# Performance work log

Hardware: AMD Instinct MI355X
Metric: run time of the kernel (lower is better)

The kernel has to match this reference:

```python
import jax, jax.numpy as jnp
import numpy as np
from jax import lax

B, N = 16, 2048
S0, S1, K = 256, 128, 32
EPS = 1e-5


def bn_relu(x, gamma, beta, axes):
    # training-mode BatchNorm (batch statistics) + ReLU; channel is last dim
    mean = jnp.mean(x, axis=axes, keepdims=True)
    var = jnp.var(x, axis=axes, keepdims=True)
    return jax.nn.relu((x - mean) * lax.rsqrt(var + EPS) * gamma + beta)


def fps(coords, s):
    # farthest point sampling, deterministic start at index 0. coords [B,N,3]
    b, n, _ = coords.shape
    def body(carry, _):
        dist, far = carry
        centroid = jnp.take_along_axis(coords, far[:, None, None], axis=1)  # [B,1,3]
        d = jnp.sum((coords - centroid) ** 2, axis=-1)                      # [B,N]
        dist = jnp.minimum(dist, d)
        return (dist, jnp.argmax(dist, axis=-1).astype(jnp.int32)), far
    init = (jnp.full((b, n), 1e10, coords.dtype), jnp.zeros((b,), jnp.int32))
    _, idx = lax.scan(body, init, None, length=s)
    return jnp.transpose(idx)  # [B,s]


def gather_points(pts, idx):
    # pts [B,N,C], idx [B,...] int -> [B,...,C]
    flat = idx.reshape(idx.shape[0], -1)[..., None]  # [B,M,1]
    out = jnp.take_along_axis(pts, flat, axis=1)     # [B,M,C]
    return out.reshape(*idx.shape, pts.shape[-1])


def sample_and_knn_group(s, k, coords, features):
    # coords [B,N,3], features [B,N,C] -> new_xyz [B,s,3], agg [B,s,k,2C]
    fps_idx = fps(coords, s)
    new_xyz = gather_points(coords, fps_idx)      # [B,s,3]
    center = gather_points(features, fps_idx)     # [B,s,C]
    d2 = jnp.sum((new_xyz[:, :, None, :] - coords[:, None, :, :]) ** 2, axis=-1)  # [B,s,N]
    _, knn_idx = lax.top_k(-d2, k)                # k smallest distances
    grouped = gather_points(features, knn_idx)    # [B,s,k,C]
    agg = jnp.concatenate(
        [grouped - center[:, :, None, :],
         jnp.broadcast_to(center[:, :, None, :], grouped.shape)], axis=-1)
    return new_xyz, agg


def sg_block(coords, features, s, k, w, gamma, beta):
    # conv1x1 -> BN -> ReLU -> max over k neighbors
    new_xyz, nf = sample_and_knn_group(s, k, coords, features)  # nf [B,s,k,d]
    h = jnp.einsum('bskd,od->bsko', nf, w)
    h = bn_relu(h, gamma, beta, axes=(0, 1, 2))
    return new_xyz, jnp.max(h, axis=2)  # [B,s,out]


def setup_inputs() -> dict:
    key = jax.random.key(0)
    ks = jax.random.split(key, 5)
    return {
        'x': jax.random.normal(ks[0], (B, 3, N), jnp.float32),
        'w1': jax.random.normal(ks[1], (64, 3), jnp.float32) * (1.0 / np.sqrt(3)),
        'g1': jnp.ones((64,), jnp.float32), 'b1': jnp.zeros((64,), jnp.float32),
        'w2': jax.random.normal(ks[2], (64, 64), jnp.float32) * 0.125,
        'g2': jnp.ones((64,), jnp.float32), 'b2': jnp.zeros((64,), jnp.float32),
        'w_sg0': jax.random.normal(ks[3], (128, 128), jnp.float32) * (1.0 / np.sqrt(128)),
        'g_sg0': jnp.ones((128,), jnp.float32), 'b_sg0': jnp.zeros((128,), jnp.float32),
        'w_sg1': jax.random.normal(ks[4], (256, 256), jnp.float32) * (1.0 / np.sqrt(256)),
        'g_sg1': jnp.ones((256,), jnp.float32), 'b_sg1': jnp.zeros((256,), jnp.float32),
    }


def reference(x, w1, g1, b1, w2, g2, b2, w_sg0, g_sg0, b_sg0, w_sg1, g_sg1, b_sg1):
    coords = jnp.transpose(x, (0, 2, 1))                   # [B,N,3]
    f = bn_relu(jnp.einsum('bnc,oc->bno', coords, w1), g1, b1, axes=(0, 1))  # [B,N,64]
    f = bn_relu(jnp.einsum('bnc,oc->bno', f, w2), g2, b2, axes=(0, 1))       # [B,N,64]
    xyz1, f1 = sg_block(coords, f, S0, K, w_sg0, g_sg0, b_sg0)   # [B,S0,128]
    _, f2 = sg_block(xyz1, f1, S1, K, w_sg1, g_sg1, b_sg1)       # [B,S1,256]
    return jnp.transpose(f2, (0, 2, 1))                           # [B,256,S1]
```

## Files before the change

### kernel.cpp

```cpp
#include <hip/hip_runtime.h>
#include <float.h>

#define BATCH 16
#define NPTS  2048
#define NS0   256
#define NS1   128
#define KK    32
#define EPSV  1e-5f
#define MROWS 32768.0f

__device__ __forceinline__ float sqdist(float ax,float ay,float az,float bx,float by,float bz){
  float dx=__fsub_rn(ax,bx), dy=__fsub_rn(ay,by), dz=__fsub_rn(az,bz);
  return __fadd_rn(__fadd_rn(__fmul_rn(dx,dx),__fmul_rn(dy,dy)),__fmul_rn(dz,dz));
}

template<int CTRL,int RM>
__device__ __forceinline__ float dpp_fmax_s(float x){
  int t = __builtin_amdgcn_update_dpp((int)0xFF800000, __float_as_int(x), CTRL, RM, 0xf, false);
  return fmaxf(x, __int_as_float(t));
}
template<int CTRL,int RM>
__device__ __forceinline__ float dpp_fmin_s(float x){
  int t = __builtin_amdgcn_update_dpp(0x7F800000, __float_as_int(x), CTRL, RM, 0xf, false);
  return fminf(x, __int_as_float(t));
}
template<int CTRL,int RM>
__device__ __forceinline__ unsigned dpp_umin_s(unsigned x){
  unsigned t = (unsigned)__builtin_amdgcn_update_dpp(-1, (int)x, CTRL, RM, 0xf, false);
  return t<x ? t : x;
}
__device__ __forceinline__ void wave_argmax_f32(float v, unsigned idx, float& mall, int& sel){
  float m=v;
  m=dpp_fmax_s<0x111,0xf>(m); m=dpp_fmax_s<0x112,0xf>(m); m=dpp_fmax_s<0x114,0xf>(m);
  m=dpp_fmax_s<0x118,0xf>(m); m=dpp_fmax_s<0x142,0xa>(m); m=dpp_fmax_s<0x143,0xc>(m);
  mall = __int_as_float(__builtin_amdgcn_readlane(__float_as_int(m),63));
  unsigned c = (v==mall)? idx : 0xFFFFFFFFu;
  c=dpp_umin_s<0x111,0xf>(c); c=dpp_umin_s<0x112,0xf>(c); c=dpp_umin_s<0x114,0xf>(c);
  c=dpp_umin_s<0x118,0xf>(c); c=dpp_umin_s<0x142,0xa>(c); c=dpp_umin_s<0x143,0xc>(c);
  sel = (int)(unsigned)__builtin_amdgcn_readlane((int)c,63);
}
__device__ __forceinline__ int wave_argmin_f32(float v, unsigned idx){
  float m=v;
  m=dpp_fmin_s<0x111,0xf>(m); m=dpp_fmin_s<0x112,0xf>(m); m=dpp_fmin_s<0x114,0xf>(m);
  m=dpp_fmin_s<0x118,0xf>(m); m=dpp_fmin_s<0x142,0xa>(m); m=dpp_fmin_s<0x143,0xc>(m);
  float mall = __int_as_float(__builtin_amdgcn_readlane(__float_as_int(m),63));
  unsigned c = (v==mall)? idx : 0xFFFFFFFFu;
  c=dpp_umin_s<0x111,0xf>(c); c=dpp_umin_s<0x112,0xf>(c); c=dpp_umin_s<0x114,0xf>(c);
  c=dpp_umin_s<0x118,0xf>(c); c=dpp_umin_s<0x142,0xa>(c); c=dpp_umin_s<0x143,0xc>(c);
  return (int)(unsigned)__builtin_amdgcn_readlane((int)c,63);
}


__device__ void embed1_body(int bid, const float* __restrict__ x, const float* __restrict__ w1,
                            float* __restrict__ coords, float* __restrict__ t1){
  __shared__ float w[64*3];
  int tid = threadIdx.x;
  if (tid < 192) w[tid] = w1[tid];
  __syncthreads();
  int gid = bid*256 + tid;
  int b = gid / NPTS, n = gid % NPTS;
  float cx = x[(b*3+0)*NPTS + n];
  float cy = x[(b*3+1)*NPTS + n];
  float cz = x[(b*3+2)*NPTS + n];
  coords[gid*3+0]=cx; coords[gid*3+1]=cy; coords[gid*3+2]=cz;
  float* o = t1 + (size_t)gid*64;
  #pragma unroll
  for(int j=0;j<64;j++) o[j] = cx*w[j*3+0] + cy*w[j*3+1] + cz*w[j*3+2];
}

__device__ void wt_body(int gid, const float* __restrict__ w0, float* __restrict__ wt0,
                        const float* __restrict__ w1, float* __restrict__ wt1){
  if(gid < 128*128){
    int o = gid % 128, c = gid / 128;
    wt0[gid] = w0[o*128 + c];
  } else {
    int g2 = gid - 128*128;
    if(g2 >= 256*256) return;
    int o = g2 % 256, c = g2 / 256;
    wt1[g2] = w1[o*256 + c];
  }
}

__device__ void statsA_body(int blk, const float* __restrict__ t,
                            float* __restrict__ accS, float* __restrict__ accQ){
  int c = threadIdx.x;
  int r0 = blk*128;
  float s=0.f, q=0.f;
  for(int r=0;r<128;r++){
    float v = t[(size_t)(r0+r)*64 + c];
    s+=v; q+=v*v;
  }
  atomicAdd(accS+c, s);
  atomicAdd(accQ+c, q);
}

__device__ void embed2_body(int bid, const float* __restrict__ t1, const float* __restrict__ w2,
                            const float* __restrict__ accS, const float* __restrict__ accQ,
                            const float* __restrict__ g1, const float* __restrict__ b1,
                            float* __restrict__ t2, char* smem){
  float (*fin)[64] = (float(*)[64])smem;
  float* sm = (float*)smem + 4096;
  float* sr = sm+64; float* sg = sr+64; float* sb = sg+64;
  int tid = threadIdx.x;
  if (tid<64){
    float S=accS[tid], Q=accQ[tid];
    float m = S/MROWS, v = Q/MROWS - m*m; if(v<0.f) v=0.f;
    sm[tid]=m; sr[tid]=rsqrtf(v+EPSV); sg[tid]=g1[tid]; sb[tid]=b1[tid];
  }
  __syncthreads();
  int base = bid*64;
  for(int i=tid;i<4096;i+=256){
    int p=i>>6, c=i&63;
    float v = t1[(size_t)(base+p)*64 + c];
    v = (v - sm[c])*sr[c]*sg[c] + sb[c];
    fin[p][c] = v>0.f ? v : 0.f;
  }
  __syncthreads();
  int o = tid & 63, p0 = tid>>6;
  float acc[16];
  #pragma unroll
  for(int i=0;i<16;i++) acc[i]=0.f;
  for(int cc=0; cc<64; cc+=4){
    float4 wv = *(const float4*)(w2 + o*64 + cc);
    #pragma unroll
    for(int i=0;i<16;i++){
      float4 f4 = *(const float4*)&fin[p0 + i*4][cc];
      acc[i] += f4.x*wv.x + f4.y*wv.y + f4.z*wv.z + f4.w*wv.w;
    }
  }
  #pragma unroll
  for(int i=0;i<16;i++) t2[(size_t)(base+p0+i*4)*64 + o] = acc[i];
}

template<int P, int S, int T>
__device__ void fps_body(int b, const float* __restrict__ x, int* __restrict__ outIdx,
                         float* __restrict__ outXyz, char* smem){
  constexpr int PPT = P/T;
  constexpr int NW  = T/64;
  float* sx=(float*)smem; float* sy=sx+P; float* sz=sy+P;
  int* sidx=(int*)(sz+P);
  unsigned long long* rv64=(unsigned long long*)(sidx+S);
  int tid = threadIdx.x;
  const float* xb = x + (size_t)b*3*P;
  float px[PPT], py[PPT], pz[PPT], dist[PPT];
  #pragma unroll
  for(int i=0;i<PPT;i++){
    int n = i*T + tid;
    float X=xb[n], Y=xb[P+n], Z=xb[2*P+n];
    px[i]=X; py[i]=Y; pz[i]=Z; dist[i]=1e10f;
    sx[n]=X; sy[n]=Y; sz[n]=Z;
  }
  __syncthreads();
  int cur = 0;
  float cx=sx[0], cy=sy[0], cz=sz[0];
  for(int s=0;s<S;s++){
    if(tid==0) sidx[s]=cur;
    if(s==S-1) break;
    float bv=-FLT_MAX; int bi=0;
    #pragma unroll
    for(int i=0;i<PPT;i++){
      float d = sqdist(px[i],py[i],pz[i],cx,cy,cz);
      float nd = fminf(dist[i], d);
      dist[i]=nd;
      int n = i*T + tid;
      if(nd>bv){ bv=nd; bi=n; }
    }
    float mall; int sel;
    wave_argmax_f32(bv,(unsigned)bi,mall,sel);
    int sl = s & 1;
    if((tid&63)==0) rv64[sl*NW+(tid>>6)] = ((unsigned long long)__float_as_uint(mall)<<32)|(unsigned)(~sel);
    __syncthreads();
    unsigned long long wk = rv64[sl*NW];
    #pragma unroll
    for(int w=1;w<NW;w++){ unsigned long long t = rv64[sl*NW+w]; if(t>wk) wk=t; }
    cur = (int)(~(unsigned)wk);
    cx=sx[cur]; cy=sy[cur]; cz=sz[cur];
  }
  __syncthreads();
  for(int i=tid; i<S; i+=T){
    int id = sidx[i];
    outIdx[b*S+i] = id;
    outXyz[((size_t)b*S+i)*3+0] = sx[id];
    outXyz[((size_t)b*S+i)*3+1] = sy[id];
    outXyz[((size_t)b*S+i)*3+2] = sz[id];
  }
}

template<int P, int S>
__device__ void fps_wave_body(int b, const float* __restrict__ pts, int* __restrict__ outIdx,
                              float* __restrict__ outXyz, char* smem){
  constexpr int PPT = P/64;
  float* sx=(float*)smem; float* sy=sx+P; float* sz=sy+P;
  int* sidx=(int*)(sz+P);
  int lane = threadIdx.x;
  const float* p = pts + (size_t)b*P*3;
  float px[PPT], py[PPT], pz[PPT], dist[PPT];
  #pragma unroll
  for(int i=0;i<PPT;i++){
    int n = i*64 + lane;
    float X=p[n*3], Y=p[n*3+1], Z=p[n*3+2];
    px[i]=X; py[i]=Y; pz[i]=Z; dist[i]=1e10f;
    sx[n]=X; sy[n]=Y; sz[n]=Z;
  }
  __syncthreads();
  int cur = 0;
  float cx=sx[0], cy=sy[0], cz=sz[0];
  for(int s=0;s<S;s++){
    if(lane==0) sidx[s]=cur;
    if(s==S-1) break;
    float bv=-FLT_MAX; int bi=0;
    #pragma unroll
    for(int i=0;i<PPT;i++){
      float d = sqdist(px[i],py[i],pz[i],cx,cy,cz);
      float nd = fminf(dist[i], d);
      dist[i]=nd;
      int n = i*64 + lane;
      if(nd>bv){ bv=nd; bi=n; }
    }
    float mall; int sel;
    wave_argmax_f32(bv,(unsigned)bi,mall,sel);
    cur = sel;
    cx=sx[cur]; cy=sy[cur]; cz=sz[cur];
  }
  __syncthreads();
  for(int i=lane; i<S; i+=64){
    int id = sidx[i];
    outIdx[b*S+i] = id;
    outXyz[((size_t)b*S+i)*3+0] = sx[id];
    outXyz[((size_t)b*S+i)*3+1] = sy[id];
    outXyz[((size_t)b*S+i)*3+2] = sz[id];
  }
}

template<int P>
__device__ void knn_body(int bq, const float* __restrict__ pts, const float* __restrict__ q,
                         int S, int* __restrict__ knn, char* smem){
  float* d2 = (float*)smem;
  constexpr int E = P/64;
  int lane = threadIdx.x;
  int b = bq / S;
  const float* p = pts + (size_t)b*P*3;
  float qx=q[(size_t)bq*3], qy=q[(size_t)bq*3+1], qz=q[(size_t)bq*3+2];
  #pragma unroll
  for(int i=0;i<E;i++){ int n=i*64+lane; d2[n] = sqdist(qx,qy,qz,p[n*3],p[n*3+1],p[n*3+2]); }
  __syncthreads();
  for(int j=0;j<KK;j++){
    float mv=FLT_MAX; unsigned mi=0xFFFFFFFFu;
    #pragma unroll
    for(int i=0;i<E;i++){
      int n=i*64+lane;
      float v=d2[n];
      if(v<mv){ mv=v; mi=(unsigned)n; }
    }
    int sel = wave_argmin_f32(mv, mi);
    if(lane==0){ knn[(size_t)bq*KK+j]=sel; d2[sel]=FLT_MAX; }
    __syncthreads();
  }
}

template<int C, int P, bool BN>
__device__ void pass1_body(int bq, const float* __restrict__ feats, const int* __restrict__ knn,
                           const int* __restrict__ fpsIdx, const float* __restrict__ WT,
                           float* __restrict__ hmax, float* __restrict__ hmin,
                           float* __restrict__ part, int S,
                           const float* __restrict__ accS, const float* __restrict__ accQ,
                           const float* __restrict__ bg, const float* __restrict__ bb){
  constexpr int O   = 2*C;
  constexpr int TPB = C;
  constexpr int C4  = C/4;
  constexpr int OG  = O/8;
  constexpr int LDC = C+4;
  __shared__ __align__(16) float gfp[KK*LDC];
  __shared__ __align__(16) float cf[C];
  __shared__ __align__(16) float sa[BN?C:1], sbb[BN?C:1];
  __shared__ float sct[O];
  __shared__ float xst[(TPB>64)? 8*O : 1];
  int tid = threadIdx.x;
  int b = bq / S;
  const float* fb = feats + (size_t)b*P*C;
  int ci = fpsIdx[bq];
  const float* cfg = fb + (size_t)ci*C;
  if(BN){
    float S_=accS[tid], Q_=accQ[tid];
    float m = S_/MROWS, vv = Q_/MROWS - m*m; if(vv<0.f) vv=0.f;
    float a = rsqrtf(vv+EPSV)*bg[tid];
    float sh = bb[tid] - m*a;
    sa[tid]=a; sbb[tid]=sh;
    float cv = a*cfg[tid] + sh;
    cf[tid] = cv>0.f ? cv : 0.f;
    __syncthreads();
  } else {
    cf[tid] = cfg[tid];
  }
  for(int i=tid; i<KK*C4; i+=TPB){
    int k = i/C4, d4 = i - k*C4;
    float4 g = ((const float4*)(fb + (size_t)knn[(size_t)bq*KK+k]*C))[d4];
    float4 r;
    if(BN){
      float4 a4 = *(const float4*)&sa[d4*4];
      float4 s4 = *(const float4*)&sbb[d4*4];
      float4 c4 = *(const float4*)&cf[d4*4];
      float gx = a4.x*g.x+s4.x; gx = gx>0.f?gx:0.f;
      float gy = a4.y*g.y+s4.y; gy = gy>0.f?gy:0.f;
      float gz = a4.z*g.z+s4.z; gz = gz>0.f?gz:0.f;
      float gw = a4.w*g.w+s4.w; gw = gw>0.f?gw:0.f;
      r.x=gx-c4.x; r.y=gy-c4.y; r.z=gz-c4.z; r.w=gw-c4.w;
    } else {
      float4 c4 = ((const float4*)cfg)[d4];
      r.x=g.x-c4.x; r.y=g.y-c4.y; r.z=g.z-c4.z; r.w=g.w-c4.w;
    }
    *(float4*)&gfp[k*LDC + d4*4] = r;
  }
  __syncthreads();
  {
    int o2 = tid*2;
    float ct0=0.f, ct1=0.f;
    for(int c=0;c<C;c+=4){
      float4 c4 = *(const float4*)&cf[c];
      #pragma unroll
      for(int t=0;t<4;t++){
        float cv = ((const float*)&c4)[t];
        float2 wh = *(const float2*)&WT[(size_t)(C+c+t)*O + o2];
        ct0 += cv*wh.x; ct1 += cv*wh.y;
      }
    }
    sct[o2]=ct0; sct[o2+1]=ct1;
  }
  __syncthreads();
  int kg = tid / OG;
  int og = tid % OG;
  float acc[8][8];
  #pragma unroll
  for(int a=0;a<8;a++)
    #pragma unroll
    for(int bb2=0;bb2<8;bb2++) acc[a][bb2]=0.f;
  for(int dc=0; dc<C4; dc++){
    float4 g4[8];
    #pragma unroll
    for(int jk=0;jk<8;jk++) g4[jk] = *(const float4*)&gfp[(kg*8+jk)*LDC + dc*4];
    #pragma unroll
    for(int t=0;t<4;t++){
      const float* wrow = WT + (size_t)(dc*4+t)*O + og*8;
      float4 wa = *(const float4*)wrow;
      float4 wb = *(const float4*)(wrow+4);
      #pragma unroll
      for(int jk=0;jk<8;jk++){
        float gs = ((const float*)&g4[jk])[t];
        acc[jk][0] += gs*wa.x; acc[jk][1] += gs*wa.y; acc[jk][2] += gs*wa.z; acc[jk][3] += gs*wa.w;
        acc[jk][4] += gs*wb.x; acc[jk][5] += gs*wb.y; acc[jk][6] += gs*wb.z; acc[jk][7] += gs*wb.w;
      }
    }
  }
  float tmx[8],tmn[8],tsm[8],tsq[8];
  #pragma unroll
  for(int jo=0;jo<8;jo++){
    int o = og*8+jo;
    float ct = sct[o];
    float s=0.f,q=0.f,mx=-FLT_MAX,mn=FLT_MAX;
    #pragma unroll
    for(int jk=0;jk<8;jk++){
      float h = acc[jk][jo] + ct;
      s+=h; q+=h*h; mx=fmaxf(mx,h); mn=fminf(mn,h);
    }
    tmx[jo]=mx; tmn[jo]=mn; tsm[jo]=s; tsq[jo]=q;
  }
  if constexpr (TPB==64){
    #pragma unroll
    for(int jo=0;jo<8;jo++){
      tmx[jo]=fmaxf(tmx[jo],__shfl_xor(tmx[jo],16)); tmx[jo]=fmaxf(tmx[jo],__shfl_xor(tmx[jo],32));
      tmn[jo]=fminf(tmn[jo],__shfl_xor(tmn[jo],16)); tmn[jo]=fminf(tmn[jo],__shfl_xor(tmn[jo],32));
      tsm[jo]+=__shfl_xor(tsm[jo],16); tsm[jo]+=__shfl_xor(tsm[jo],32);
      tsq[jo]+=__shfl_xor(tsq[jo],16); tsq[jo]+=__shfl_xor(tsq[jo],32);
    }
    if(tid<OG){
      #pragma unroll
      for(int jo=0;jo<8;jo++){
        int o = tid*8+jo;
        hmax[(size_t)bq*O+o]=tmx[jo]; hmin[(size_t)bq*O+o]=tmn[jo];
        part[(size_t)bq*2*O+o]=tsm[jo]; part[(size_t)bq*2*O+O+o]=tsq[jo];
      }
    }
  } else {
    #pragma unroll
    for(int jo=0;jo<8;jo++){
      tmx[jo]=fmaxf(tmx[jo],__shfl_xor(tmx[jo],32));
      tmn[jo]=fminf(tmn[jo],__shfl_xor(tmn[jo],32));
      tsm[jo]+=__shfl_xor(tsm[jo],32);
      tsq[jo]+=__shfl_xor(tsq[jo],32);
    }
    int wv = tid>>6;
    if((tid&63)<32){
      int og_ = tid&31;
      #pragma unroll
      for(int jo=0;jo<8;jo++){
        int o = og_*8+jo;
        xst[0*2*O + wv*O + o]=tmx[jo];
        xst[1*2*O + wv*O + o]=tmn[jo];
        xst[2*2*O + wv*O + o]=tsm[jo];
        xst[3*2*O + wv*O + o]=tsq[jo];
      }
    }
    __syncthreads();
    if(tid<32){
      #pragma unroll
      for(int jo=0;jo<8;jo++){
        int o = tid*8+jo;
        hmax[(size_t)bq*O+o]=fmaxf(xst[0*2*O+o], xst[0*2*O+O+o]);
        hmin[(size_t)bq*O+o]=fminf(xst[1*2*O+o], xst[1*2*O+O+o]);
        part[(size_t)bq*2*O+o]   = xst[2*2*O+o] + xst[2*2*O+O+o];
        part[(size_t)bq*2*O+O+o] = xst[3*2*O+o] + xst[3*2*O+O+o];
      }
    }
  }
}


__global__ __launch_bounds__(256) void k_embed1_wt(const float* __restrict__ x, const float* __restrict__ w1,
                         float* __restrict__ coords, float* __restrict__ t1,
                         const float* __restrict__ wsg0, float* __restrict__ wt0,
                         const float* __restrict__ wsg1, float* __restrict__ wt1,
                         float* __restrict__ accz){
  if(blockIdx.x < 128) embed1_body(blockIdx.x, x, w1, coords, t1);
  else if(blockIdx.x < 448) wt_body((blockIdx.x-128)*256 + threadIdx.x, wsg0, wt0, wsg1, wt1);
  else accz[threadIdx.x] = 0.f;
}

__global__ __launch_bounds__(64) void k_statsA(const float* __restrict__ t,
                         float* __restrict__ accS, float* __restrict__ accQ){
  statsA_body(blockIdx.x, t, accS, accQ);
}

__global__ __launch_bounds__(256, 1) void k_fps0_embed2(const float* __restrict__ x,
                         int* __restrict__ fps0, float* __restrict__ xyz0,
                         const float* __restrict__ t1, const float* __restrict__ w2,
                         const float* __restrict__ acc1S, const float* __restrict__ acc1Q,
                         const float* __restrict__ g1, const float* __restrict__ b1,
                         float* __restrict__ t2){
  extern __shared__ char smem[];
  if(blockIdx.x < BATCH) fps_body<NPTS,NS0,256>(blockIdx.x, x, fps0, xyz0, smem);
  else embed2_body(blockIdx.x-BATCH, t1, w2, acc1S, acc1Q, g1, b1, t2, smem);
}

__global__ __launch_bounds__(64, 4) void k_fps1_knn0_st2(const float* __restrict__ xyz0,
                         int* __restrict__ fps1, float* __restrict__ xyz1,
                         const float* __restrict__ coords, int* __restrict__ knn0,
                         const float* __restrict__ t2,
                         float* __restrict__ acc2S, float* __restrict__ acc2Q){
  extern __shared__ char smem[];
  if(blockIdx.x < BATCH) fps_wave_body<NS0,NS1>(blockIdx.x, xyz0, fps1, xyz1, smem);
  else if(blockIdx.x < BATCH + BATCH*NS0) knn_body<NPTS>(blockIdx.x-BATCH, coords, xyz0, NS0, knn0, smem);
  else statsA_body(blockIdx.x - (BATCH + BATCH*NS0), t2, acc2S, acc2Q);
}

__global__ __launch_bounds__(64, 2) void k_pass1a_knn1(const float* __restrict__ t2,
                         const int* __restrict__ knn0, const int* __restrict__ fps0,
                         const float* __restrict__ wt0,
                         float* __restrict__ hmax0, float* __restrict__ hmin0, float* __restrict__ part0,
                         const float* __restrict__ acc2S, const float* __restrict__ acc2Q,
                         const float* __restrict__ g2, const float* __restrict__ b2,
                         const float* __restrict__ xyz0, const float* __restrict__ xyz1,
                         int* __restrict__ knn1){
  extern __shared__ char smem[];
  if(blockIdx.x < BATCH*NS0)
    pass1_body<64,NPTS,true>(blockIdx.x, t2, knn0, fps0, wt0, hmax0, hmin0, part0, NS0,
                             acc2S, acc2Q, g2, b2);
  else
    knn_body<NS0>(blockIdx.x-BATCH*NS0, xyz0, xyz1, NS1, knn1, smem);
}

__global__ __launch_bounds__(128, 2) void k_pass1b(const float* __restrict__ f1,
                         const int* __restrict__ knn1, const int* __restrict__ fps1,
                         const float* __restrict__ wt1,
                         float* __restrict__ hmax1, float* __restrict__ hmin1, float* __restrict__ part1){
  pass1_body<128,NS0,false>(blockIdx.x, f1, knn1, fps1, wt1, hmax1, hmin1, part1, NS1,
                            nullptr, nullptr, nullptr, nullptr);
}

__global__ __launch_bounds__(256) void k_redpost0(const float* __restrict__ part,
        const float* __restrict__ hmax, const float* __restrict__ hmin,
        const float* __restrict__ g, const float* __restrict__ bb, float* __restrict__ f1){
  constexpr int O=128; constexpr int NB=BATCH*NS0;
  int o = blockIdx.x, tid = threadIdx.x;
  float s=0.f, s2=0.f;
  for(int i=tid;i<NB;i+=256){ s += part[(size_t)i*2*O+o]; s2 += part[(size_t)i*2*O+O+o]; }
  __shared__ float bs[256], bq[256];
  __shared__ float s_sc, s_sh;
  bs[tid]=s; bq[tid]=s2; __syncthreads();
  for(int st=128; st>0; st>>=1){ if(tid<st){ bs[tid]+=bs[tid+st]; bq[tid]+=bq[tid+st]; } __syncthreads(); }
  if(tid==0){
    float M = (float)(NB*KK);
    float m = bs[0]/M;
    float v = bq[0]/M - m*m; if(v<0.f) v=0.f;
    float sc = rsqrtf(v+EPSV)*g[o];
    s_sc = sc; s_sh = bb[o] - m*sc;
  }
  __syncthreads();
  float sc=s_sc, sh=s_sh;
  const float* hs = (sc>=0.f) ? hmax : hmin;
  for(int r=tid; r<NB; r+=256){
    float v = hs[(size_t)r*O+o]*sc + sh;
    f1[(size_t)r*O+o] = v>0.f ? v : 0.f;
  }
}

__global__ __launch_bounds__(256) void k_redpost1(const float* __restrict__ part,
        const float* __restrict__ hmax, const float* __restrict__ hmin,
        const float* __restrict__ g, const float* __restrict__ bb, float* __restrict__ out){
  constexpr int O=256; constexpr int NB=BATCH*NS1;
  int o = blockIdx.x, tid = threadIdx.x;
  float s=0.f, s2=0.f;
  for(int i=tid;i<NB;i+=256){ s += part[(size_t)i*2*O+o]; s2 += part[(size_t)i*2*O+O+o]; }
  __shared__ float bs[256], bq[256];
  __shared__ float s_sc, s_sh;
  bs[tid]=s; bq[tid]=s2; __syncthreads();
  for(int st=128; st>0; st>>=1){ if(tid<st){ bs[tid]+=bs[tid+st]; bq[tid]+=bq[tid+st]; } __syncthreads(); }
  if(tid==0){
    float M = (float)(NB*KK);
    float m = bs[0]/M;
    float v = bq[0]/M - m*m; if(v<0.f) v=0.f;
    float sc = rsqrtf(v+EPSV)*g[o];
    s_sc = sc; s_sh = bb[o] - m*sc;
  }
  __syncthreads();
  float sc=s_sc, sh=s_sh;
  const float* hs = (sc>=0.f) ? hmax : hmin;
  for(int r=tid; r<NB; r+=256){
    float v = hs[(size_t)r*O+o]*sc + sh;
    v = v>0.f ? v : 0.f;
    int b = r>>7, ss = r&(NS1-1);
    out[(size_t)b*(256*NS1) + o*NS1 + ss] = v;
  }
}

extern "C" void kernel_launch(void* const* d_in, const int* in_sizes, int n_in,
                              void* d_out, int out_size, void* d_ws, size_t ws_size,
                              hipStream_t stream){
  const float* x    = (const float*)d_in[0];
  const float* w1   = (const float*)d_in[1];
  const float* g1   = (const float*)d_in[2];
  const float* b1   = (const float*)d_in[3];
  const float* w2   = (const float*)d_in[4];
  const float* g2   = (const float*)d_in[5];
  const float* b2   = (const float*)d_in[6];
  const float* wsg0 = (const float*)d_in[7];
  const float* gsg0 = (const float*)d_in[8];
  const float* bsg0 = (const float*)d_in[9];
  const float* wsg1 = (const float*)d_in[10];
  const float* gsg1 = (const float*)d_in[11];
  const float* bsg1 = (const float*)d_in[12];
  float* out = (float*)d_out;

  float* wsf = (float*)d_ws;
  float* coords = wsf;                    wsf += BATCH*NPTS*3;
  float* t1     = wsf;                    wsf += BATCH*NPTS*64;
  float* t2     = wsf;                    wsf += BATCH*NPTS*64;
  float* acc1S=wsf; wsf+=64;  float* acc1Q=wsf; wsf+=64;
  float* acc2S=wsf; wsf+=64;  float* acc2Q=wsf; wsf+=64;
  int*   fps0 = (int*)wsf;                wsf += BATCH*NS0;
  float* xyz0 = wsf;                      wsf += BATCH*NS0*3;
  int*   knn0 = (int*)wsf;                wsf += BATCH*NS0*KK;
  float* hmax0= wsf;                      wsf += BATCH*NS0*128;
  float* hmin0= wsf;                      wsf += BATCH*NS0*128;
  float* part0= wsf;                      wsf += BATCH*NS0*2*128;
  float* f1   = wsf;                      wsf += BATCH*NS0*128;
  int*   fps1 = (int*)wsf;                wsf += BATCH*NS1;
  float* xyz1 = wsf;                      wsf += BATCH*NS1*3;
  int*   knn1 = (int*)wsf;                wsf += BATCH*NS1*KK;
  float* hmax1= wsf;                      wsf += BATCH*NS1*256;
  float* hmin1= wsf;                      wsf += BATCH*NS1*256;
  float* part1= wsf;                      wsf += BATCH*NS1*2*256;
  float* wt0  = wsf;                      wsf += 128*128;
  float* wt1  = wsf;                      wsf += 256*256;

  const int DYN_L3 = (NPTS*3 + NS0)*4 + 2*4*8;
  const int DYN_L4 = NPTS*4;
  const int DYN_L5 = NS0*4;

  k_embed1_wt<<<dim3(449), dim3(256), 0, stream>>>(x, w1, coords, t1, wsg0, wt0, wsg1, wt1, acc1S);
  k_statsA<<<dim3(256), dim3(64), 0, stream>>>(t1, acc1S, acc1Q);
  k_fps0_embed2<<<dim3(BATCH+512), dim3(256), DYN_L3, stream>>>(x, fps0, xyz0,
                                                  t1, w2, acc1S, acc1Q, g1, b1, t2);
  k_fps1_knn0_st2<<<dim3(BATCH + BATCH*NS0 + 256), dim3(64), DYN_L4, stream>>>(
                                                  xyz0, fps1, xyz1, coords, knn0, t2, acc2S, acc2Q);
  k_pass1a_knn1<<<dim3(BATCH*NS0 + BATCH*NS1), dim3(64), DYN_L5, stream>>>(t2, knn0, fps0, wt0,
                                                  hmax0, hmin0, part0,
                                                  acc2S, acc2Q, g2, b2,
                                                  xyz0, xyz1, knn1);
  k_redpost0<<<dim3(128), dim3(256), 0, stream>>>(part0, hmax0, hmin0, gsg0, bsg0, f1);
  k_pass1b<<<dim3(BATCH*NS1), dim3(128), 0, stream>>>(f1, knn1, fps1, wt1, hmax1, hmin1, part1);
  k_redpost1<<<dim3(256), dim3(256), 0, stream>>>(part1, hmax1, hmin1, gsg1, bsg1, out);
}
```

Measured before the change: 415.5 us.

## Coalesce embed stores, register-resident KNN, split BN reductions into atomic stats plus elementwise post

The embed kernel now stages a 64-point tile in shared memory so the t1 writes are coalesced. The KNN selection keeps its distances in registers and rescans only in the lane that owns the selected point, removing the shared-memory rescan and a barrier on every step. FPS stores points as float4 in LDS. The per-channel BN reduction kernels are replaced by column-sum kernels that use atomics, plus elementwise post kernels; stage 1 uses a shared-memory transposed output tile. pass1b writes per-wave partials, which removes its LDS cross-wave merge, and it reuses the t1/t2 buffers. This adds launches, and the atomics make the sums order-nondeterministic.

```diff
diff --git a/kernel.cpp b/kernel.cpp
--- a/kernel.cpp
+++ b/kernel.cpp
@@ -53,19 +53,35 @@
 
 __device__ void embed1_body(int bid, const float* __restrict__ x, const float* __restrict__ w1,
                             float* __restrict__ coords, float* __restrict__ t1){
-  __shared__ float w[64*3];
+  __shared__ float w[192];
+  __shared__ float xs[3][64];
+  __shared__ float fin[64][65];
   int tid = threadIdx.x;
   if (tid < 192) w[tid] = w1[tid];
-  __syncthreads();
-  int gid = bid*256 + tid;
-  int b = gid / NPTS, n = gid % NPTS;
-  float cx = x[(b*3+0)*NPTS + n];
-  float cy = x[(b*3+1)*NPTS + n];
-  float cz = x[(b*3+2)*NPTS + n];
-  coords[gid*3+0]=cx; coords[gid*3+1]=cy; coords[gid*3+2]=cz;
-  float* o = t1 + (size_t)gid*64;
-  #pragma unroll
-  for(int j=0;j<64;j++) o[j] = cx*w[j*3+0] + cy*w[j*3+1] + cz*w[j*3+2];
+  int base = bid*64;
+  int b = base / NPTS, n0 = base % NPTS;
+  if (tid < 192){
+    int ch = tid>>6, i = tid&63;
+    xs[ch][i] = x[((size_t)b*3+ch)*NPTS + n0 + i];
+  }
+  __syncthreads();
+  if (tid < 64){
+    coords[(size_t)(base+tid)*3+0]=xs[0][tid];
+    coords[(size_t)(base+tid)*3+1]=xs[1][tid];
+    coords[(size_t)(base+tid)*3+2]=xs[2][tid];
+  }
+  int p = tid>>2, c0 = (tid&3)<<4;
+  float cx=xs[0][p], cy=xs[1][p], cz=xs[2][p];
+  #pragma unroll
+  for(int j=0;j<16;j++){
+    int c = c0+j;
+    fin[p][c] = cx*w[c*3+0] + cy*w[c*3+1] + cz*w[c*3+2];
+  }
+  __syncthreads();
+  for(int i=tid;i<4096;i+=256){
+    int pp=i>>6, c=i&63;
+    t1[(size_t)base*64 + i] = fin[pp][c];
+  }
 }
 
 __device__ void wt_body(int gid, const float* __restrict__ w0, float* __restrict__ wt0,
@@ -190,8 +206,8 @@
 __device__ void fps_wave_body(int b, const float* __restrict__ pts, int* __restrict__ outIdx,
                               float* __restrict__ outXyz, char* smem){
   constexpr int PPT = P/64;
-  float* sx=(float*)smem; float* sy=sx+P; float* sz=sy+P;
-  int* sidx=(int*)(sz+P);
+  float4* sp = (float4*)smem;
+  int* sidx = (int*)(smem + P*sizeof(float4));
   int lane = threadIdx.x;
   const float* p = pts + (size_t)b*P*3;
   float px[PPT], py[PPT], pz[PPT], dist[PPT];
@@ -200,11 +216,11 @@
     int n = i*64 + lane;
     float X=p[n*3], Y=p[n*3+1], Z=p[n*3+2];
     px[i]=X; py[i]=Y; pz[i]=Z; dist[i]=1e10f;
-    sx[n]=X; sy[n]=Y; sz[n]=Z;
+    sp[n] = make_float4(X,Y,Z,0.f);
   }
   __syncthreads();
   int cur = 0;
-  float cx=sx[0], cy=sy[0], cz=sz[0];
+  float cx=sp[0].x, cy=sp[0].y, cz=sp[0].z;
   for(int s=0;s<S;s++){
     if(lane==0) sidx[s]=cur;
     if(s==S-1) break;
@@ -220,41 +236,51 @@
     float mall; int sel;
     wave_argmax_f32(bv,(unsigned)bi,mall,sel);
     cur = sel;
-    cx=sx[cur]; cy=sy[cur]; cz=sz[cur];
+    float4 cp = sp[cur];
+    cx=cp.x; cy=cp.y; cz=cp.z;
   }
   __syncthreads();
   for(int i=lane; i<S; i+=64){
     int id = sidx[i];
+    float4 cp = sp[id];
     outIdx[b*S+i] = id;
-    outXyz[((size_t)b*S+i)*3+0] = sx[id];
-    outXyz[((size_t)b*S+i)*3+1] = sy[id];
-    outXyz[((size_t)b*S+i)*3+2] = sz[id];
+    outXyz[((size_t)b*S+i)*3+0] = cp.x;
+    outXyz[((size_t)b*S+i)*3+1] = cp.y;
+    outXyz[((size_t)b*S+i)*3+2] = cp.z;
   }
 }
 
 template<int P>
 __device__ void knn_body(int bq, const float* __restrict__ pts, const float* __restrict__ q,
-                         int S, int* __restrict__ knn, char* smem){
-  float* d2 = (float*)smem;
+                         int S, int* __restrict__ knn){
   constexpr int E = P/64;
   int lane = threadIdx.x;
   int b = bq / S;
   const float* p = pts + (size_t)b*P*3;
   float qx=q[(size_t)bq*3], qy=q[(size_t)bq*3+1], qz=q[(size_t)bq*3+2];
-  #pragma unroll
-  for(int i=0;i<E;i++){ int n=i*64+lane; d2[n] = sqdist(qx,qy,qz,p[n*3],p[n*3+1],p[n*3+2]); }
-  __syncthreads();
+  float dl[E];
+  float mv = FLT_MAX; unsigned mi = 0xFFFFFFFFu;
+  #pragma unroll
+  for(int i=0;i<E;i++){
+    int n = i*64 + lane;
+    float v = sqdist(qx,qy,qz,p[n*3],p[n*3+1],p[n*3+2]);
+    dl[i] = v;
+    if(v<mv){ mv=v; mi=(unsigned)n; }
+  }
   for(int j=0;j<KK;j++){
-    float mv=FLT_MAX; unsigned mi=0xFFFFFFFFu;
-    #pragma unroll
-    for(int i=0;i<E;i++){
-      int n=i*64+lane;
-      float v=d2[n];
-      if(v<mv){ mv=v; mi=(unsigned)n; }
-    }
     int sel = wave_argmin_f32(mv, mi);
-    if(lane==0){ knn[(size_t)bq*KK+j]=sel; d2[sel]=FLT_MAX; }
-    __syncthreads();
+    if(lane==0) knn[(size_t)bq*KK+j] = sel;
+    if((sel & 63) == lane){
+      int slot = sel >> 6;
+      #pragma unroll
+      for(int i=0;i<E;i++) if(i==slot) dl[i]=FLT_MAX;
+      mv = FLT_MAX; mi = 0xFFFFFFFFu;
+      #pragma unroll
+      for(int i=0;i<E;i++){
+        int n=i*64+lane;
+        if(dl[i]<mv){ mv=dl[i]; mi=(unsigned)n; }
+      }
+    }
   }
 }
 
@@ -274,7 +300,6 @@
   __shared__ __align__(16) float cf[C];
   __shared__ __align__(16) float sa[BN?C:1], sbb[BN?C:1];
   __shared__ float sct[O];
-  __shared__ float xst[(TPB>64)? 8*O : 1];
   int tid = threadIdx.x;
   int b = bq / S;
   const float* fb = feats + (size_t)b*P*C;
@@ -391,24 +416,12 @@
     int wv = tid>>6;
     if((tid&63)<32){
       int og_ = tid&31;
+      size_t rb = (size_t)bq*2 + wv;
       #pragma unroll
       for(int jo=0;jo<8;jo++){
         int o = og_*8+jo;
-        xst[0*2*O + wv*O + o]=tmx[jo];
-        xst[1*2*O + wv*O + o]=tmn[jo];
-        xst[2*2*O + wv*O + o]=tsm[jo];
-        xst[3*2*O + wv*O + o]=tsq[jo];
-      }
-    }
-    __syncthreads();
-    if(tid<32){
-      #pragma unroll
-      for(int jo=0;jo<8;jo++){
-        int o = tid*8+jo;
-        hmax[(size_t)bq*O+o]=fmaxf(xst[0*2*O+o], xst[0*2*O+O+o]);
-        hmin[(size_t)bq*O+o]=fminf(xst[1*2*O+o], xst[1*2*O+O+o]);
-        part[(size_t)bq*2*O+o]   = xst[2*2*O+o] + xst[2*2*O+O+o];
-        part[(size_t)bq*2*O+O+o] = xst[3*2*O+o] + xst[3*2*O+O+o];
+        hmax[rb*O+o]=tmx[jo]; hmin[rb*O+o]=tmn[jo];
+        part[rb*2*O+o]=tsm[jo]; part[rb*2*O+O+o]=tsq[jo];
       }
     }
   }
@@ -420,9 +433,12 @@
                          const float* __restrict__ wsg0, float* __restrict__ wt0,
                          const float* __restrict__ wsg1, float* __restrict__ wt1,
                          float* __restrict__ accz){
-  if(blockIdx.x < 128) embed1_body(blockIdx.x, x, w1, coords, t1);
-  else if(blockIdx.x < 448) wt_body((blockIdx.x-128)*256 + threadIdx.x, wsg0, wt0, wsg1, wt1);
-  else accz[threadIdx.x] = 0.f;
+  if(blockIdx.x < 512) embed1_body(blockIdx.x, x, w1, coords, t1);
+  else if(blockIdx.x < 832) wt_body((blockIdx.x-512)*256 + threadIdx.x, wsg0, wt0, wsg1, wt1);
+  else {
+    int tid = threadIdx.x;
+    accz[tid]=0.f; accz[tid+256]=0.f; accz[tid+512]=0.f; accz[tid+768]=0.f;
+  }
 }
 
 __global__ __launch_bounds__(64) void k_statsA(const float* __restrict__ t,
@@ -448,7 +464,7 @@
                          float* __restrict__ acc2S, float* __restrict__ acc2Q){
   extern __shared__ char smem[];
   if(blockIdx.x < BATCH) fps_wave_body<NS0,NS1>(blockIdx.x, xyz0, fps1, xyz1, smem);
-  else if(blockIdx.x < BATCH + BATCH*NS0) knn_body<NPTS>(blockIdx.x-BATCH, coords, xyz0, NS0, knn0, smem);
+  else if(blockIdx.x < BATCH + BATCH*NS0) knn_body<NPTS>(blockIdx.x-BATCH, coords, xyz0, NS0, knn0);
   else statsA_body(blockIdx.x - (BATCH + BATCH*NS0), t2, acc2S, acc2Q);
 }
 
@@ -460,12 +476,11 @@
                          const float* __restrict__ g2, const float* __restrict__ b2,
                          const float* __restrict__ xyz0, const float* __restrict__ xyz1,
                          int* __restrict__ knn1){
-  extern __shared__ char smem[];
   if(blockIdx.x < BATCH*NS0)
     pass1_body<64,NPTS,true>(blockIdx.x, t2, knn0, fps0, wt0, hmax0, hmin0, part0, NS0,
                              acc2S, acc2Q, g2, b2);
   else
-    knn_body<NS0>(blockIdx.x-BATCH*NS0, xyz0, xyz1, NS1, knn1, smem);
+    knn_body<NS0>(blockIdx.x-BATCH*NS0, xyz0, xyz1, NS1, knn1);
 }
 
 __global__ __launch_bounds__(128, 2) void k_pass1b(const float* __restrict__ f1,
@@ -476,59 +491,66 @@
                             nullptr, nullptr, nullptr, nullptr);
 }
 
-__global__ __launch_bounds__(256) void k_redpost0(const float* __restrict__ part,
-        const float* __restrict__ hmax, const float* __restrict__ hmin,
+__global__ __launch_bounds__(256) void k_statsB(const float* __restrict__ part, int W,
+                                                float* __restrict__ acc){
+  int tid = threadIdx.x;
+  int r0 = blockIdx.x*64;
+  for(int c=tid; c<W; c+=256){
+    float a=0.f;
+    for(int r=0;r<64;r++) a += part[(size_t)(r0+r)*W + c];
+    atomicAdd(acc+c, a);
+  }
+}
+
+__global__ __launch_bounds__(256) void k_postmax0(const float* __restrict__ hmax, const float* __restrict__ hmin,
+        const float* __restrict__ aS, const float* __restrict__ aQ,
         const float* __restrict__ g, const float* __restrict__ bb, float* __restrict__ f1){
-  constexpr int O=128; constexpr int NB=BATCH*NS0;
-  int o = blockIdx.x, tid = threadIdx.x;
-  float s=0.f, s2=0.f;
-  for(int i=tid;i<NB;i+=256){ s += part[(size_t)i*2*O+o]; s2 += part[(size_t)i*2*O+O+o]; }
-  __shared__ float bs[256], bq[256];
-  __shared__ float s_sc, s_sh;
-  bs[tid]=s; bq[tid]=s2; __syncthreads();
-  for(int st=128; st>0; st>>=1){ if(tid<st){ bs[tid]+=bs[tid+st]; bq[tid]+=bq[tid+st]; } __syncthreads(); }
-  if(tid==0){
-    float M = (float)(NB*KK);
-    float m = bs[0]/M;
-    float v = bq[0]/M - m*m; if(v<0.f) v=0.f;
+  __shared__ float ssc[128], ssh[128];
+  int tid = threadIdx.x;
+  if(tid<128){
+    float M = (float)(BATCH*NS0*KK);
+    float m = aS[tid]/M, v = aQ[tid]/M - m*m; if(v<0.f) v=0.f;
+    float sc = rsqrtf(v+EPSV)*g[tid];
+    ssc[tid]=sc; ssh[tid]=bb[tid]-m*sc;
+  }
+  __syncthreads();
+  int idx = blockIdx.x*256 + tid;
+  int o = idx & 127;
+  float sc=ssc[o];
+  float h = (sc>=0.f) ? hmax[idx] : hmin[idx];
+  float v = h*sc + ssh[o];
+  f1[idx] = v>0.f ? v : 0.f;
+}
+
+__global__ __launch_bounds__(256) void k_post1tr(const float* __restrict__ hmax, const float* __restrict__ hmin,
+        const float* __restrict__ aS, const float* __restrict__ aQ,
+        const float* __restrict__ g, const float* __restrict__ bb, float* __restrict__ out){
+  __shared__ float ssc[64], ssh[64];
+  __shared__ float tile[64][129];
+  int tid = threadIdx.x;
+  int blk = blockIdx.x; int b = blk>>2; int c0 = (blk&3)*64;
+  if(tid<64){
+    int o = c0+tid;
+    float M = (float)(BATCH*NS1*KK);
+    float m = aS[o]/M, v = aQ[o]/M - m*m; if(v<0.f) v=0.f;
     float sc = rsqrtf(v+EPSV)*g[o];
-    s_sc = sc; s_sh = bb[o] - m*sc;
-  }
-  __syncthreads();
-  float sc=s_sc, sh=s_sh;
-  const float* hs = (sc>=0.f) ? hmax : hmin;
-  for(int r=tid; r<NB; r+=256){
-    float v = hs[(size_t)r*O+o]*sc + sh;
-    f1[(size_t)r*O+o] = v>0.f ? v : 0.f;
-  }
-}
-
-__global__ __launch_bounds__(256) void k_redpost1(const float* __restrict__ part,
-        const float* __restrict__ hmax, const float* __restrict__ hmin,
-        const float* __restrict__ g, const float* __restrict__ bb, float* __restrict__ out){
-  constexpr int O=256; constexpr int NB=BATCH*NS1;
-  int o = blockIdx.x, tid = threadIdx.x;
-  float s=0.f, s2=0.f;
-  for(int i=tid;i<NB;i+=256){ s += part[(size_t)i*2*O+o]; s2 += part[(size_t)i*2*O+O+o]; }
-  __shared__ float bs[256], bq[256];
-  __shared__ float s_sc, s_sh;
-  bs[tid]=s; bq[tid]=s2; __syncthreads();
-  for(int st=128; st>0; st>>=1){ if(tid<st){ bs[tid]+=bs[tid+st]; bq[tid]+=bq[tid+st]; } __syncthreads(); }
-  if(tid==0){
-    float M = (float)(NB*KK);
-    float m = bs[0]/M;
-    float v = bq[0]/M - m*m; if(v<0.f) v=0.f;
-    float sc = rsqrtf(v+EPSV)*g[o];
-    s_sc = sc; s_sh = bb[o] - m*sc;
-  }
-  __syncthreads();
-  float sc=s_sc, sh=s_sh;
-  const float* hs = (sc>=0.f) ? hmax : hmin;
-  for(int r=tid; r<NB; r+=256){
-    float v = hs[(size_t)r*O+o]*sc + sh;
-    v = v>0.f ? v : 0.f;
-    int b = r>>7, ss = r&(NS1-1);
-    out[(size_t)b*(256*NS1) + o*NS1 + ss] = v;
+    ssc[tid]=sc; ssh[tid]=bb[o]-m*sc;
+  }
+  __syncthreads();
+  for(int i=tid; i<128*64; i+=256){
+    int r=i>>6, ch=i&63;
+    size_t rb = (size_t)(b*NS1+r)*2;
+    float sc = ssc[ch];
+    float va = hmax[rb*256 + c0+ch], vb = hmax[(rb+1)*256 + c0+ch];
+    float wa = hmin[rb*256 + c0+ch], wb = hmin[(rb+1)*256 + c0+ch];
+    float h = (sc>=0.f) ? fmaxf(va,vb) : fminf(wa,wb);
+    float v = h*sc + ssh[ch];
+    tile[ch][r] = v>0.f ? v : 0.f;
+  }
+  __syncthreads();
+  for(int i=tid; i<64*128; i+=256){
+    int ch=i>>7, s=i&127;
+    out[(size_t)b*(256*NS1) + (size_t)(c0+ch)*NS1 + s] = tile[ch][s];
   }
 }
 
@@ -556,6 +578,8 @@
   float* t2     = wsf;                    wsf += BATCH*NPTS*64;
   float* acc1S=wsf; wsf+=64;  float* acc1Q=wsf; wsf+=64;
   float* acc2S=wsf; wsf+=64;  float* acc2Q=wsf; wsf+=64;
+  float* accB0=wsf; wsf+=256;
+  float* accB1=wsf; wsf+=512;
   int*   fps0 = (int*)wsf;                wsf += BATCH*NS0;
   float* xyz0 = wsf;                      wsf += BATCH*NS0*3;
   int*   knn0 = (int*)wsf;                wsf += BATCH*NS0*KK;
@@ -566,27 +590,28 @@
   int*   fps1 = (int*)wsf;                wsf += BATCH*NS1;
   float* xyz1 = wsf;                      wsf += BATCH*NS1*3;
   int*   knn1 = (int*)wsf;                wsf += BATCH*NS1*KK;
-  float* hmax1= wsf;                      wsf += BATCH*NS1*256;
-  float* hmin1= wsf;                      wsf += BATCH*NS1*256;
-  float* part1= wsf;                      wsf += BATCH*NS1*2*256;
   float* wt0  = wsf;                      wsf += 128*128;
   float* wt1  = wsf;                      wsf += 256*256;
+  float* part1 = t1;
+  float* hmax1 = t2;
+  float* hmin1 = t2 + BATCH*NS1*2*256;
 
   const int DYN_L3 = (NPTS*3 + NS0)*4 + 2*4*8;
-  const int DYN_L4 = NPTS*4;
-  const int DYN_L5 = NS0*4;
-
-  k_embed1_wt<<<dim3(449), dim3(256), 0, stream>>>(x, w1, coords, t1, wsg0, wt0, wsg1, wt1, acc1S);
+  const int DYN_L4 = NS0*16 + NS1*4;
+
+  k_embed1_wt<<<dim3(833), dim3(256), 0, stream>>>(x, w1, coords, t1, wsg0, wt0, wsg1, wt1, acc1S);
   k_statsA<<<dim3(256), dim3(64), 0, stream>>>(t1, acc1S, acc1Q);
   k_fps0_embed2<<<dim3(BATCH+512), dim3(256), DYN_L3, stream>>>(x, fps0, xyz0,
                                                   t1, w2, acc1S, acc1Q, g1, b1, t2);
   k_fps1_knn0_st2<<<dim3(BATCH + BATCH*NS0 + 256), dim3(64), DYN_L4, stream>>>(
                                                   xyz0, fps1, xyz1, coords, knn0, t2, acc2S, acc2Q);
-  k_pass1a_knn1<<<dim3(BATCH*NS0 + BATCH*NS1), dim3(64), DYN_L5, stream>>>(t2, knn0, fps0, wt0,
+  k_pass1a_knn1<<<dim3(BATCH*NS0 + BATCH*NS1), dim3(64), 0, stream>>>(t2, knn0, fps0, wt0,
                                                   hmax0, hmin0, part0,
                                                   acc2S, acc2Q, g2, b2,
                                                   xyz0, xyz1, knn1);
-  k_redpost0<<<dim3(128), dim3(256), 0, stream>>>(part0, hmax0, hmin0, gsg0, bsg0, f1);
+  k_statsB<<<dim3(64), dim3(256), 0, stream>>>(part0, 256, accB0);
+  k_postmax0<<<dim3(2048), dim3(256), 0, stream>>>(hmax0, hmin0, accB0, accB0+128, gsg0, bsg0, f1);
   k_pass1b<<<dim3(BATCH*NS1), dim3(128), 0, stream>>>(f1, knn1, fps1, wt1, hmax1, hmin1, part1);
-  k_redpost1<<<dim3(256), dim3(256), 0, stream>>>(part1, hmax1, hmin1, gsg1, bsg1, out);
-}
+  k_statsB<<<dim3(64), dim3(256), 0, stream>>>(part1, 512, accB1);
+  k_post1tr<<<dim3(64), dim3(256), 0, stream>>>(hmax1, hmin1, accB1, accB1+256, gsg1, bsg1, out);
+}
```

New measurement: 410.3 us. About the same (-1.2%).
